# Kernel tuning notes

Measured on AMD Instinct MI355X. Metric: run time of the kernel, lower is better.

The kernel has to match this reference:

```python
import jax, jax.numpy as jnp
import numpy as np

SPATIAL_W = 1.0
INTENSITY_W = 1.0
MAX_ITERS = 100
CONV_THRESH = 1e-4
BOUNDARY = 0.1
NUM_CLASSES = 2
DIRS = ((-1, 0), (1, 0), (0, -1), (0, 1))  # 4-neighborhood


def setup_inputs() -> dict:
    key = jax.random.key(0)
    k1, k2, k3 = jax.random.split(key, 3)
    H = W = 1024
    image = jax.random.uniform(k1, (H, W), dtype=jnp.float32)
    labels = jax.random.randint(k2, (H, W), 1, NUM_CLASSES + 1)
    u = jax.random.uniform(k3, (H, W))
    seeds = jnp.where(u < 0.002, labels, 0).astype(jnp.int32)
    # guarantee both classes present (torch code maps sorted unique labels -> class idx)
    seeds = seeds.at[0, 0].set(1).at[0, 1].set(2)
    return {"image": image, "seeds": seeds}


def _shift(x, di, dj):
    """out[i, j] = x[i+di, j+dj] if in-bounds else 0. Static di, dj in {-1,0,1}."""
    H, W = x.shape[0], x.shape[1]
    pad = [(1, 1), (1, 1)] + [(0, 0)] * (x.ndim - 2)
    xp = jnp.pad(x, pad)
    return xp[1 + di:1 + di + H, 1 + dj:1 + dj + W]


def _transition_stencil(image):
    """Row-normalized 4-neighbor transition weights, [4, H, W].
    Equivalent to the dense NxN matrix P of the torch code restricted to its
    nonzero 4-neighbor stencil."""
    img = image[..., None]  # [H, W, 1] (grayscale -> C=1)
    ones = jnp.ones(image.shape, image.dtype)
    ws = []
    for di, dj in DIRS:
        valid = _shift(ones, di, dj)              # 1 where neighbor in-bounds
        nb = _shift(img, di, dj)                   # neighbor pixel values
        same = ((img > BOUNDARY) ^ (nb > BOUNDARY)).astype(image.dtype)
        diff = img - nb + same
        intensity = jnp.sqrt(jnp.sum(diff * diff, axis=-1))  # per-channel L2 norm
        dist = float(np.sqrt(di * di + dj * dj))  # == 1 for 4-neighborhood
        w = jnp.exp(-SPATIAL_W * dist) * jnp.exp(-INTENSITY_W * intensity) * valid
        ws.append(w)
    ws = jnp.stack(ws)  # [4, H, W]
    rowsum = jnp.sum(ws, axis=0)
    rowsum = jnp.where(rowsum == 0, jnp.ones_like(rowsum), rowsum)
    return ws / rowsum


def reference(image, seeds):
    P = _transition_stencil(image)  # [4, H, W]
    seed_mask = (seeds > 0)[..., None]  # [H, W, 1]
    # one-hot seed probabilities: label l -> class l-1 (sorted unique labels {1,2})
    init = jnp.stack([seeds == l for l in range(1, NUM_CLASSES + 1)],
                     axis=-1).astype(image.dtype)  # [H, W, C]

    def matvec(x):  # (P @ x) as a stencil: x is [H, W, C]
        out = jnp.zeros_like(x)
        for d, (di, dj) in enumerate(DIRS):
            out = out + P[d][..., None] * _shift(x, di, dj)
        return out

    def step(carry, _):
        x, done = carry
        new = jnp.where(seed_mask, init, matvec(x))  # seeds are absorbing
        d = jnp.linalg.norm(new - x)
        new = jnp.where(done, x, new)               # freeze after convergence
        done = done | (d < CONV_THRESH)
        return (new, done), None

    (x, _), _ = jax.lax.scan(step, (init, jnp.array(False)), None, length=MAX_ITERS)
    return x  # [H, W, NUM_CLASSES]
```

## Files before the change

kernel.cpp:

```cpp
#include <hip/hip_runtime.h>
#include <hip/hip_fp16.h>

typedef __attribute__((ext_vector_type(2))) int i32x2;

#define HH 1024
#define ROWP 512
#define NBLK 256
#define TPB 512
#define NSYNC 50
#define BOUNDARY_F 0.1f
#define TOKEN 0x5A5A5A5Au
#define FLAGS_N (NSYNC * NBLK)

union h2u { __half2 h; int i; };

__device__ __forceinline__ i32x2 pack4(float4 v) {
    h2u a, b;
    a.h = __float22half2_rn(make_float2(v.x, v.y));
    b.h = __float22half2_rn(make_float2(v.z, v.w));
    i32x2 r; r.x = a.i; r.y = b.i;
    return r;
}
__device__ __forceinline__ float4 unpack4(i32x2 p) {
    h2u a, b; a.i = p.x; b.i = p.y;
    float2 lo = __half22float2(a.h);
    float2 hi = __half22float2(b.h);
    return make_float4(lo.x, lo.y, hi.x, hi.y);
}

__device__ __forceinline__ void cst8(i32x2* base, int elem, i32x2 val) {
    asm volatile("global_store_dwordx2 %0, %1, %2 sc0 sc1"
                 :: "v"(elem * 8), "v"(val), "s"(base) : "memory");
}
__device__ __forceinline__ i32x2 cld8(const i32x2* base, int elem) {
    i32x2 t;
    asm volatile("global_load_dwordx2 %0, %1, %2 sc0 sc1"
                 : "=v"(t) : "v"(elem * 8), "s"(base) : "memory");
    return t;
}
__device__ __forceinline__ void wait4(i32x2& a, i32x2& b, i32x2& c, i32x2& d) {
    asm volatile("s_waitcnt vmcnt(0)"
                 : "+v"(a), "+v"(b), "+v"(c), "+v"(d) :: "memory");
}
__device__ __forceinline__ void waitvm0() {
    asm volatile("s_waitcnt vmcnt(0)" ::: "memory");
}

__device__ __forceinline__ float wfun(float c, float n, float valid) {
    float same = ((c > BOUNDARY_F) != (n > BOUNDARY_F)) ? 1.0f : 0.0f;
    return valid * __expf(-fabsf(c - n + same));
}

__device__ __forceinline__ float4 stepr(const float* w, bool m0, bool m1,
                                        float4 xc, float4 xu, float4 xd,
                                        float2 xl, float2 xr) {
    float4 o;
    o.x = w[0]*xu.x + w[1]*xd.x + w[2]*xl.x + w[3]*xc.z;
    o.y = w[0]*xu.y + w[1]*xd.y + w[2]*xl.y + w[3]*xc.w;
    o.z = w[4]*xu.z + w[5]*xd.z + w[6]*xc.x + w[7]*xr.x;
    o.w = w[4]*xu.w + w[5]*xd.w + w[6]*xc.y + w[7]*xr.y;
    if (m0) { o.x = xc.x; o.y = xc.y; }
    if (m1) { o.z = xc.z; o.w = xc.w; }
    return o;
}

__device__ __forceinline__ void horiz(const float4* row, int tid, float4 xc,
                                      float2* xl, float2* xr) {
    const float2* r2 = (const float2*)row;
    *xl = (tid > 0) ? r2[2 * tid - 1] : make_float2(xc.x, xc.y);
    *xr = (tid < ROWP - 1) ? r2[2 * tid + 2] : make_float2(xc.z, xc.w);
}

__global__ void rw_init_kernel(unsigned* __restrict__ flags) {
    int g = blockIdx.x * blockDim.x + threadIdx.x;
    if (g < FLAGS_N) flags[g] = 0u;
}

__launch_bounds__(TPB)
__global__ void rw_persist_kernel(const float* __restrict__ img,
                                  const int* __restrict__ seeds,
                                  float4* __restrict__ out4,
                                  i32x2* __restrict__ parE,
                                  i32x2* __restrict__ parO,
                                  unsigned* __restrict__ flags) {
    const int tid = threadIdx.x;
    const int blk = blockIdx.x;
    const int band = ((blk & 7) << 5) | (blk >> 3);
    const int i0 = band * 4;

    __shared__ float4 srows[10][ROWP];

    float cfv[6][8];
    unsigned mb0 = 0, mb1 = 0;
    float4 s0, s1, s2, s3;
    {
        const float2* img2 = (const float2*)img;
        const int2* seeds2 = (const int2*)seeds;
#pragma unroll
        for (int L = 0; L < 6; ++L) {
            const int g = min(max(i0 - 1 + L, 0), HH - 1);
            const int P = g * ROWP + tid;
            const int p = P * 2;
            const int j = p & 1023;
            const int uP = (g > 0) ? P - ROWP : P;
            const int dP = (g < HH - 1) ? P + ROWP : P;
            const int lp = (j > 0) ? p - 1 : p;
            const int rp = (j < 1022) ? p + 2 : p + 1;

            float2 cc = img2[P], iu = img2[uP], id = img2[dP];
            float il = img[lp], ir = img[rp];
            const float vU = (g > 0) ? 1.0f : 0.0f;
            const float vD = (g < HH - 1) ? 1.0f : 0.0f;
            const float vL = (j > 0) ? 1.0f : 0.0f;
            const float vR = (j < 1022) ? 1.0f : 0.0f;

            float w0u = wfun(cc.x, iu.x, vU), w0d = wfun(cc.x, id.x, vD);
            float w0l = wfun(cc.x, il, vL),   w0r = wfun(cc.x, cc.y, 1.0f);
            float rs0 = w0u + w0d + w0l + w0r;
            float inv0 = (rs0 > 0.0f) ? 1.0f / rs0 : 0.0f;
            float w1u = wfun(cc.y, iu.y, vU), w1d = wfun(cc.y, id.y, vD);
            float w1l = wfun(cc.y, cc.x, 1.0f), w1r = wfun(cc.y, ir, vR);
            float rs1 = w1u + w1d + w1l + w1r;
            float inv1 = (rs1 > 0.0f) ? 1.0f / rs1 : 0.0f;

            cfv[L][0] = w0u * inv0; cfv[L][1] = w0d * inv0;
            cfv[L][2] = w0l * inv0; cfv[L][3] = w0r * inv0;
            cfv[L][4] = w1u * inv1; cfv[L][5] = w1d * inv1;
            cfv[L][6] = w1l * inv1; cfv[L][7] = w1r * inv1;

            int2 s = seeds2[P];
            if (s.x > 0) mb0 |= 1u << L;
            if (s.y > 0) mb1 |= 1u << L;
            if (L >= 1 && L <= 4) {
                float4 v;
                v.x = (s.x == 1) ? 1.0f : 0.0f;
                v.y = (s.x == 2) ? 1.0f : 0.0f;
                v.z = (s.y == 1) ? 1.0f : 0.0f;
                v.w = (s.y == 2) ? 1.0f : 0.0f;
                if (L == 1) s0 = v; else if (L == 2) s1 = v;
                else if (L == 3) s2 = v; else s3 = v;
            }
        }
    }

    srows[1][tid] = s0; srows[2][tid] = s1;
    srows[3][tid] = s2; srows[4][tid] = s3;
    cst8(parE, (i0 + 0) * ROWP + tid, pack4(s0));
    cst8(parE, (i0 + 1) * ROWP + tid, pack4(s1));
    cst8(parE, (i0 + 2) * ROWP + tid, pack4(s2));
    cst8(parE, (i0 + 3) * ROWP + tid, pack4(s3));
    waitvm0();
    __syncthreads();
    if (tid == 0)
        __hip_atomic_store(&flags[band], TOKEN, __ATOMIC_RELAXED,
                           __HIP_MEMORY_SCOPE_AGENT);

    const int gU2 = max(i0 - 2, 0), gU1 = max(i0 - 1, 0);
    const int gD0 = min(i0 + 4, HH - 1), gD1 = min(i0 + 5, HH - 1);

    for (int m = 0; m < NSYNC; ++m) {
        if (tid == 0 && band > 0) {
            int guard = 0;
            while (__hip_atomic_load(&flags[m * NBLK + band - 1], __ATOMIC_RELAXED,
                                     __HIP_MEMORY_SCOPE_AGENT) != TOKEN) {
                if (++guard > (1 << 22)) break;
            }
        }
        if (tid == 64 && band < NBLK - 1) {
            int guard = 0;
            while (__hip_atomic_load(&flags[m * NBLK + band + 1], __ATOMIC_RELAXED,
                                     __HIP_MEMORY_SCOPE_AGENT) != TOKEN) {
                if (++guard > (1 << 22)) break;
            }
        }
        __syncthreads();
        asm volatile("" ::: "memory");

        const i32x2* pin = (m & 1) ? parO : parE;

        i32x2 rA = cld8(pin, gU2 * ROWP + tid);
        i32x2 rB = cld8(pin, gU1 * ROWP + tid);
        i32x2 rC = cld8(pin, gD0 * ROWP + tid);
        i32x2 rD = cld8(pin, gD1 * ROWP + tid);

        float2 xl, xr;
        horiz(&srows[2][0], tid, s1, &xl, &xr);
        float4 y2 = stepr(cfv[2], (mb0 >> 2) & 1, (mb1 >> 2) & 1, s1, s0, s2, xl, xr);
        horiz(&srows[3][0], tid, s2, &xl, &xr);
        float4 y3 = stepr(cfv[3], (mb0 >> 3) & 1, (mb1 >> 3) & 1, s2, s1, s3, xl, xr);
        srows[7][tid] = y2;
        srows[8][tid] = y3;

        wait4(rA, rB, rC, rD);
        float4 vU2 = unpack4(rA);
        float4 vU1 = unpack4(rB);
        float4 vD0 = unpack4(rC);
        float4 vD1 = unpack4(rD);
        srows[0][tid] = vU1;
        srows[5][tid] = vD0;
        __syncthreads();

        horiz(&srows[0][0], tid, vU1, &xl, &xr);
        float4 y0 = stepr(cfv[0], (mb0 >> 0) & 1, (mb1 >> 0) & 1, vU1, vU2, s0, xl, xr);
        horiz(&srows[1][0], tid, s0, &xl, &xr);
        float4 y1 = stepr(cfv[1], (mb0 >> 1) & 1, (mb1 >> 1) & 1, s0, vU1, s1, xl, xr);
        horiz(&srows[4][0], tid, s3, &xl, &xr);
        float4 y4 = stepr(cfv[4], (mb0 >> 4) & 1, (mb1 >> 4) & 1, s3, s2, vD0, xl, xr);
        horiz(&srows[5][0], tid, vD0, &xl, &xr);
        float4 y5 = stepr(cfv[5], (mb0 >> 5) & 1, (mb1 >> 5) & 1, vD0, s3, vD1, xl, xr);
        srows[6][tid] = y1;
        srows[9][tid] = y4;
        __syncthreads();

        i32x2* pout = (m & 1) ? parE : parO;
        const bool last = (m == NSYNC - 1);

        horiz(&srows[6][0], tid, y1, &xl, &xr);
        float4 o0 = stepr(cfv[1], (mb0 >> 1) & 1, (mb1 >> 1) & 1, y1, y0, y2, xl, xr);
        if (!last) cst8(pout, (i0 + 0) * ROWP + tid, pack4(o0));
        horiz(&srows[7][0], tid, y2, &xl, &xr);
        float4 o1 = stepr(cfv[2], (mb0 >> 2) & 1, (mb1 >> 2) & 1, y2, y1, y3, xl, xr);
        if (!last) cst8(pout, (i0 + 1) * ROWP + tid, pack4(o1));
        horiz(&srows[8][0], tid, y3, &xl, &xr);
        float4 o2 = stepr(cfv[3], (mb0 >> 3) & 1, (mb1 >> 3) & 1, y3, y2, y4, xl, xr);
        if (!last) cst8(pout, (i0 + 2) * ROWP + tid, pack4(o2));
        horiz(&srows[9][0], tid, y4, &xl, &xr);
        float4 o3 = stepr(cfv[4], (mb0 >> 4) & 1, (mb1 >> 4) & 1, y4, y3, y5, xl, xr);
        if (!last) cst8(pout, (i0 + 3) * ROWP + tid, pack4(o3));

        if (last) {
            out4[(i0 + 0) * ROWP + tid] = o0;
            out4[(i0 + 1) * ROWP + tid] = o1;
            out4[(i0 + 2) * ROWP + tid] = o2;
            out4[(i0 + 3) * ROWP + tid] = o3;
            break;
        }

        waitvm0();
        __syncthreads();
        if (tid == 0)
            __hip_atomic_store(&flags[(m + 1) * NBLK + band], TOKEN,
                               __ATOMIC_RELAXED, __HIP_MEMORY_SCOPE_AGENT);

        srows[1][tid] = o0; srows[2][tid] = o1;
        srows[3][tid] = o2; srows[4][tid] = o3;
        s0 = o0; s1 = o1; s2 = o2; s3 = o3;
    }
}

extern "C" void kernel_launch(void* const* d_in, const int* in_sizes, int n_in,
                              void* d_out, int out_size, void* d_ws, size_t ws_size,
                              hipStream_t stream) {
    const float* img = (const float*)d_in[0];
    const int* seeds = (const int*)d_in[1];

    float4* out4 = (float4*)d_out;
    char* ws = (char*)d_ws;
    i32x2* parE = (i32x2*)ws;
    i32x2* parO = (i32x2*)(ws + 4ull * 1024 * 1024);
    unsigned* flags = (unsigned*)(ws + 8ull * 1024 * 1024);

    rw_init_kernel<<<(FLAGS_N + 255) / 256, 256, 0, stream>>>(flags);
    rw_persist_kernel<<<NBLK, TPB, 0, stream>>>(img, seeds, out4, parE, parO, flags);
}
```

Measured before the change: 240.6 us.

## Deepen temporal blocking to four steps per inter-block sync with wider halo

Each block now loads a 4-row halo above and below its band and advances four Jacobi steps per exchange instead of two, which halves the number of inter-block flag synchronisations from 50 to 25. The goal is to cut the global sync and halo round-trip latency that dominates the persistent kernel. In exchange it does redundant halo computation (more stencil rows per sync), uses more registers for ten coefficient rows, and needs extra shared memory and barriers per round.

```diff
diff --git a/kernel.cpp b/kernel.cpp
--- a/kernel.cpp
+++ b/kernel.cpp
@@ -7,7 +7,7 @@
 #define ROWP 512
 #define NBLK 256
 #define TPB 512
-#define NSYNC 50
+#define NSYNC 25
 #define BOUNDARY_F 0.1f
 #define TOKEN 0x5A5A5A5Au
 #define FLAGS_N (NSYNC * NBLK)
@@ -38,9 +38,11 @@
                  : "=v"(t) : "v"(elem * 8), "s"(base) : "memory");
     return t;
 }
-__device__ __forceinline__ void wait4(i32x2& a, i32x2& b, i32x2& c, i32x2& d) {
+__device__ __forceinline__ void wait8(i32x2& a, i32x2& b, i32x2& c, i32x2& d,
+                                      i32x2& e, i32x2& f, i32x2& g, i32x2& h) {
     asm volatile("s_waitcnt vmcnt(0)"
-                 : "+v"(a), "+v"(b), "+v"(c), "+v"(d) :: "memory");
+                 : "+v"(a), "+v"(b), "+v"(c), "+v"(d),
+                   "+v"(e), "+v"(f), "+v"(g), "+v"(h) :: "memory");
 }
 __device__ __forceinline__ void waitvm0() {
     asm volatile("s_waitcnt vmcnt(0)" ::: "memory");
@@ -88,17 +90,18 @@
     const int band = ((blk & 7) << 5) | (blk >> 3);
     const int i0 = band * 4;
 
-    __shared__ float4 srows[10][ROWP];
-
-    float cfv[6][8];
+    __shared__ float4 bufA[10][ROWP];
+    __shared__ float4 bufB[8][ROWP];
+
+    float cfv[10][8];
     unsigned mb0 = 0, mb1 = 0;
     float4 s0, s1, s2, s3;
     {
         const float2* img2 = (const float2*)img;
         const int2* seeds2 = (const int2*)seeds;
 #pragma unroll
-        for (int L = 0; L < 6; ++L) {
-            const int g = min(max(i0 - 1 + L, 0), HH - 1);
+        for (int L = 1; L <= 10; ++L) {
+            const int g = min(max(i0 - 4 + L, 0), HH - 1);
             const int P = g * ROWP + tid;
             const int p = P * 2;
             const int j = p & 1023;
@@ -123,28 +126,28 @@
             float rs1 = w1u + w1d + w1l + w1r;
             float inv1 = (rs1 > 0.0f) ? 1.0f / rs1 : 0.0f;
 
-            cfv[L][0] = w0u * inv0; cfv[L][1] = w0d * inv0;
-            cfv[L][2] = w0l * inv0; cfv[L][3] = w0r * inv0;
-            cfv[L][4] = w1u * inv1; cfv[L][5] = w1d * inv1;
-            cfv[L][6] = w1l * inv1; cfv[L][7] = w1r * inv1;
+            cfv[L-1][0] = w0u * inv0; cfv[L-1][1] = w0d * inv0;
+            cfv[L-1][2] = w0l * inv0; cfv[L-1][3] = w0r * inv0;
+            cfv[L-1][4] = w1u * inv1; cfv[L-1][5] = w1d * inv1;
+            cfv[L-1][6] = w1l * inv1; cfv[L-1][7] = w1r * inv1;
 
             int2 s = seeds2[P];
             if (s.x > 0) mb0 |= 1u << L;
             if (s.y > 0) mb1 |= 1u << L;
-            if (L >= 1 && L <= 4) {
+            if (L >= 4 && L <= 7) {
                 float4 v;
                 v.x = (s.x == 1) ? 1.0f : 0.0f;
                 v.y = (s.x == 2) ? 1.0f : 0.0f;
                 v.z = (s.y == 1) ? 1.0f : 0.0f;
                 v.w = (s.y == 2) ? 1.0f : 0.0f;
-                if (L == 1) s0 = v; else if (L == 2) s1 = v;
-                else if (L == 3) s2 = v; else s3 = v;
+                if (L == 4) s0 = v; else if (L == 5) s1 = v;
+                else if (L == 6) s2 = v; else s3 = v;
             }
         }
     }
 
-    srows[1][tid] = s0; srows[2][tid] = s1;
-    srows[3][tid] = s2; srows[4][tid] = s3;
+    bufA[3][tid] = s0; bufA[4][tid] = s1;
+    bufA[5][tid] = s2; bufA[6][tid] = s3;
     cst8(parE, (i0 + 0) * ROWP + tid, pack4(s0));
     cst8(parE, (i0 + 1) * ROWP + tid, pack4(s1));
     cst8(parE, (i0 + 2) * ROWP + tid, pack4(s2));
@@ -155,8 +158,10 @@
         __hip_atomic_store(&flags[band], TOKEN, __ATOMIC_RELAXED,
                            __HIP_MEMORY_SCOPE_AGENT);
 
-    const int gU2 = max(i0 - 2, 0), gU1 = max(i0 - 1, 0);
+    const int gU0 = max(i0 - 4, 0), gU1 = max(i0 - 3, 0);
+    const int gU2 = max(i0 - 2, 0), gU3 = max(i0 - 1, 0);
     const int gD0 = min(i0 + 4, HH - 1), gD1 = min(i0 + 5, HH - 1);
+    const int gD2 = min(i0 + 6, HH - 1), gD3 = min(i0 + 7, HH - 1);
 
     for (int m = 0; m < NSYNC; ++m) {
         if (tid == 0 && band > 0) {
@@ -178,54 +183,106 @@
 
         const i32x2* pin = (m & 1) ? parO : parE;
 
-        i32x2 rA = cld8(pin, gU2 * ROWP + tid);
+        i32x2 rA = cld8(pin, gU0 * ROWP + tid);
         i32x2 rB = cld8(pin, gU1 * ROWP + tid);
-        i32x2 rC = cld8(pin, gD0 * ROWP + tid);
-        i32x2 rD = cld8(pin, gD1 * ROWP + tid);
+        i32x2 rC = cld8(pin, gU2 * ROWP + tid);
+        i32x2 rD = cld8(pin, gU3 * ROWP + tid);
+        i32x2 rE = cld8(pin, gD0 * ROWP + tid);
+        i32x2 rF = cld8(pin, gD1 * ROWP + tid);
+        i32x2 rG = cld8(pin, gD2 * ROWP + tid);
+        i32x2 rH = cld8(pin, gD3 * ROWP + tid);
 
         float2 xl, xr;
-        horiz(&srows[2][0], tid, s1, &xl, &xr);
-        float4 y2 = stepr(cfv[2], (mb0 >> 2) & 1, (mb1 >> 2) & 1, s1, s0, s2, xl, xr);
-        horiz(&srows[3][0], tid, s2, &xl, &xr);
-        float4 y3 = stepr(cfv[3], (mb0 >> 3) & 1, (mb1 >> 3) & 1, s2, s1, s3, xl, xr);
-        srows[7][tid] = y2;
-        srows[8][tid] = y3;
-
-        wait4(rA, rB, rC, rD);
-        float4 vU2 = unpack4(rA);
-        float4 vU1 = unpack4(rB);
-        float4 vD0 = unpack4(rC);
-        float4 vD1 = unpack4(rD);
-        srows[0][tid] = vU1;
-        srows[5][tid] = vD0;
-        __syncthreads();
-
-        horiz(&srows[0][0], tid, vU1, &xl, &xr);
-        float4 y0 = stepr(cfv[0], (mb0 >> 0) & 1, (mb1 >> 0) & 1, vU1, vU2, s0, xl, xr);
-        horiz(&srows[1][0], tid, s0, &xl, &xr);
-        float4 y1 = stepr(cfv[1], (mb0 >> 1) & 1, (mb1 >> 1) & 1, s0, vU1, s1, xl, xr);
-        horiz(&srows[4][0], tid, s3, &xl, &xr);
-        float4 y4 = stepr(cfv[4], (mb0 >> 4) & 1, (mb1 >> 4) & 1, s3, s2, vD0, xl, xr);
-        horiz(&srows[5][0], tid, vD0, &xl, &xr);
-        float4 y5 = stepr(cfv[5], (mb0 >> 5) & 1, (mb1 >> 5) & 1, vD0, s3, vD1, xl, xr);
-        srows[6][tid] = y1;
-        srows[9][tid] = y4;
+        horiz(&bufA[4][0], tid, s1, &xl, &xr);
+        float4 y1_5 = stepr(cfv[4], (mb0 >> 5) & 1, (mb1 >> 5) & 1, s1, s0, s2, xl, xr);
+        horiz(&bufA[5][0], tid, s2, &xl, &xr);
+        float4 y1_6 = stepr(cfv[5], (mb0 >> 6) & 1, (mb1 >> 6) & 1, s2, s1, s3, xl, xr);
+        bufB[3][tid] = y1_5;
+        bufB[4][tid] = y1_6;
+
+        wait8(rA, rB, rC, rD, rE, rF, rG, rH);
+        float4 x0_0  = unpack4(rA);
+        float4 x0_1  = unpack4(rB);
+        float4 x0_2  = unpack4(rC);
+        float4 x0_3  = unpack4(rD);
+        float4 x0_8  = unpack4(rE);
+        float4 x0_9  = unpack4(rF);
+        float4 x0_10 = unpack4(rG);
+        float4 x0_11 = unpack4(rH);
+        bufA[0][tid] = x0_1; bufA[1][tid] = x0_2; bufA[2][tid] = x0_3;
+        bufA[7][tid] = x0_8; bufA[8][tid] = x0_9; bufA[9][tid] = x0_10;
+        __syncthreads();
+
+        horiz(&bufA[0][0], tid, x0_1, &xl, &xr);
+        float4 y1_1 = stepr(cfv[0], (mb0 >> 1) & 1, (mb1 >> 1) & 1, x0_1, x0_0, x0_2, xl, xr);
+        horiz(&bufA[1][0], tid, x0_2, &xl, &xr);
+        float4 y1_2 = stepr(cfv[1], (mb0 >> 2) & 1, (mb1 >> 2) & 1, x0_2, x0_1, x0_3, xl, xr);
+        horiz(&bufA[2][0], tid, x0_3, &xl, &xr);
+        float4 y1_3 = stepr(cfv[2], (mb0 >> 3) & 1, (mb1 >> 3) & 1, x0_3, x0_2, s0, xl, xr);
+        horiz(&bufA[3][0], tid, s0, &xl, &xr);
+        float4 y1_4 = stepr(cfv[3], (mb0 >> 4) & 1, (mb1 >> 4) & 1, s0, x0_3, s1, xl, xr);
+        horiz(&bufA[6][0], tid, s3, &xl, &xr);
+        float4 y1_7 = stepr(cfv[6], (mb0 >> 7) & 1, (mb1 >> 7) & 1, s3, s2, x0_8, xl, xr);
+        horiz(&bufA[7][0], tid, x0_8, &xl, &xr);
+        float4 y1_8 = stepr(cfv[7], (mb0 >> 8) & 1, (mb1 >> 8) & 1, x0_8, s3, x0_9, xl, xr);
+        horiz(&bufA[8][0], tid, x0_9, &xl, &xr);
+        float4 y1_9 = stepr(cfv[8], (mb0 >> 9) & 1, (mb1 >> 9) & 1, x0_9, x0_8, x0_10, xl, xr);
+        horiz(&bufA[9][0], tid, x0_10, &xl, &xr);
+        float4 y1_10 = stepr(cfv[9], (mb0 >> 10) & 1, (mb1 >> 10) & 1, x0_10, x0_9, x0_11, xl, xr);
+        bufB[0][tid] = y1_2; bufB[1][tid] = y1_3; bufB[2][tid] = y1_4;
+        bufB[5][tid] = y1_7; bufB[6][tid] = y1_8; bufB[7][tid] = y1_9;
+        __syncthreads();
+
+        horiz(&bufB[0][0], tid, y1_2, &xl, &xr);
+        float4 y2_2 = stepr(cfv[1], (mb0 >> 2) & 1, (mb1 >> 2) & 1, y1_2, y1_1, y1_3, xl, xr);
+        horiz(&bufB[1][0], tid, y1_3, &xl, &xr);
+        float4 y2_3 = stepr(cfv[2], (mb0 >> 3) & 1, (mb1 >> 3) & 1, y1_3, y1_2, y1_4, xl, xr);
+        horiz(&bufB[2][0], tid, y1_4, &xl, &xr);
+        float4 y2_4 = stepr(cfv[3], (mb0 >> 4) & 1, (mb1 >> 4) & 1, y1_4, y1_3, y1_5, xl, xr);
+        horiz(&bufB[3][0], tid, y1_5, &xl, &xr);
+        float4 y2_5 = stepr(cfv[4], (mb0 >> 5) & 1, (mb1 >> 5) & 1, y1_5, y1_4, y1_6, xl, xr);
+        horiz(&bufB[4][0], tid, y1_6, &xl, &xr);
+        float4 y2_6 = stepr(cfv[5], (mb0 >> 6) & 1, (mb1 >> 6) & 1, y1_6, y1_5, y1_7, xl, xr);
+        horiz(&bufB[5][0], tid, y1_7, &xl, &xr);
+        float4 y2_7 = stepr(cfv[6], (mb0 >> 7) & 1, (mb1 >> 7) & 1, y1_7, y1_6, y1_8, xl, xr);
+        horiz(&bufB[6][0], tid, y1_8, &xl, &xr);
+        float4 y2_8 = stepr(cfv[7], (mb0 >> 8) & 1, (mb1 >> 8) & 1, y1_8, y1_7, y1_9, xl, xr);
+        horiz(&bufB[7][0], tid, y1_9, &xl, &xr);
+        float4 y2_9 = stepr(cfv[8], (mb0 >> 9) & 1, (mb1 >> 9) & 1, y1_9, y1_8, y1_10, xl, xr);
+        bufA[0][tid] = y2_3; bufA[1][tid] = y2_4; bufA[2][tid] = y2_5;
+        bufA[3][tid] = y2_6; bufA[4][tid] = y2_7; bufA[5][tid] = y2_8;
+        __syncthreads();
+
+        horiz(&bufA[0][0], tid, y2_3, &xl, &xr);
+        float4 y3_3 = stepr(cfv[2], (mb0 >> 3) & 1, (mb1 >> 3) & 1, y2_3, y2_2, y2_4, xl, xr);
+        horiz(&bufA[1][0], tid, y2_4, &xl, &xr);
+        float4 y3_4 = stepr(cfv[3], (mb0 >> 4) & 1, (mb1 >> 4) & 1, y2_4, y2_3, y2_5, xl, xr);
+        horiz(&bufA[2][0], tid, y2_5, &xl, &xr);
+        float4 y3_5 = stepr(cfv[4], (mb0 >> 5) & 1, (mb1 >> 5) & 1, y2_5, y2_4, y2_6, xl, xr);
+        horiz(&bufA[3][0], tid, y2_6, &xl, &xr);
+        float4 y3_6 = stepr(cfv[5], (mb0 >> 6) & 1, (mb1 >> 6) & 1, y2_6, y2_5, y2_7, xl, xr);
+        horiz(&bufA[4][0], tid, y2_7, &xl, &xr);
+        float4 y3_7 = stepr(cfv[6], (mb0 >> 7) & 1, (mb1 >> 7) & 1, y2_7, y2_6, y2_8, xl, xr);
+        horiz(&bufA[5][0], tid, y2_8, &xl, &xr);
+        float4 y3_8 = stepr(cfv[7], (mb0 >> 8) & 1, (mb1 >> 8) & 1, y2_8, y2_7, y2_9, xl, xr);
+        bufB[0][tid] = y3_4; bufB[1][tid] = y3_5;
+        bufB[2][tid] = y3_6; bufB[3][tid] = y3_7;
         __syncthreads();
 
         i32x2* pout = (m & 1) ? parE : parO;
         const bool last = (m == NSYNC - 1);
 
-        horiz(&srows[6][0], tid, y1, &xl, &xr);
-        float4 o0 = stepr(cfv[1], (mb0 >> 1) & 1, (mb1 >> 1) & 1, y1, y0, y2, xl, xr);
+        horiz(&bufB[0][0], tid, y3_4, &xl, &xr);
+        float4 o0 = stepr(cfv[3], (mb0 >> 4) & 1, (mb1 >> 4) & 1, y3_4, y3_3, y3_5, xl, xr);
         if (!last) cst8(pout, (i0 + 0) * ROWP + tid, pack4(o0));
-        horiz(&srows[7][0], tid, y2, &xl, &xr);
-        float4 o1 = stepr(cfv[2], (mb0 >> 2) & 1, (mb1 >> 2) & 1, y2, y1, y3, xl, xr);
+        horiz(&bufB[1][0], tid, y3_5, &xl, &xr);
+        float4 o1 = stepr(cfv[4], (mb0 >> 5) & 1, (mb1 >> 5) & 1, y3_5, y3_4, y3_6, xl, xr);
         if (!last) cst8(pout, (i0 + 1) * ROWP + tid, pack4(o1));
-        horiz(&srows[8][0], tid, y3, &xl, &xr);
-        float4 o2 = stepr(cfv[3], (mb0 >> 3) & 1, (mb1 >> 3) & 1, y3, y2, y4, xl, xr);
+        horiz(&bufB[2][0], tid, y3_6, &xl, &xr);
+        float4 o2 = stepr(cfv[5], (mb0 >> 6) & 1, (mb1 >> 6) & 1, y3_6, y3_5, y3_7, xl, xr);
         if (!last) cst8(pout, (i0 + 2) * ROWP + tid, pack4(o2));
-        horiz(&srows[9][0], tid, y4, &xl, &xr);
-        float4 o3 = stepr(cfv[4], (mb0 >> 4) & 1, (mb1 >> 4) & 1, y4, y3, y5, xl, xr);
+        horiz(&bufB[3][0], tid, y3_7, &xl, &xr);
+        float4 o3 = stepr(cfv[6], (mb0 >> 7) & 1, (mb1 >> 7) & 1, y3_7, y3_6, y3_8, xl, xr);
         if (!last) cst8(pout, (i0 + 3) * ROWP + tid, pack4(o3));
 
         if (last) {
@@ -242,8 +299,8 @@
             __hip_atomic_store(&flags[(m + 1) * NBLK + band], TOKEN,
                                __ATOMIC_RELAXED, __HIP_MEMORY_SCOPE_AGENT);
 
-        srows[1][tid] = o0; srows[2][tid] = o1;
-        srows[3][tid] = o2; srows[4][tid] = o3;
+        bufA[3][tid] = o0; bufA[4][tid] = o1;
+        bufA[5][tid] = o2; bufA[6][tid] = o3;
         s0 = o0; s1 = o1; s2 = o2; s3 = o3;
     }
 }
```

After: 365.2 us. +51.8%, slower.

## Deepen temporal blocking to four steps per global sync with wavefront schedule

Applied to the files above, without the earlier changes.

Each block now exchanges a 4-row halo on each side and advances four Jacobi steps per inter-block synchronization instead of two, halving the number of global flag handshakes. The redundant halo rows are computed in a staggered wavefront through rotating shared-memory buffers. To keep register pressure manageable, the per-pixel transition weights are stored packed as fp16, and the right/left weight is recomputed from the row-sum-to-one identity. This adds redundant halo compute, more barriers per sync, and extra fp16 rounding of the coefficients.

```diff
diff --git a/kernel.cpp b/kernel.cpp
--- a/kernel.cpp
+++ b/kernel.cpp
@@ -7,7 +7,7 @@
 #define ROWP 512
 #define NBLK 256
 #define TPB 512
-#define NSYNC 50
+#define NSYNC 25
 #define BOUNDARY_F 0.1f
 #define TOKEN 0x5A5A5A5Au
 #define FLAGS_N (NSYNC * NBLK)
@@ -27,6 +27,13 @@
     float2 hi = __half22float2(b.h);
     return make_float4(lo.x, lo.y, hi.x, hi.y);
 }
+__device__ __forceinline__ unsigned packh2(float a, float b) {
+    h2u u; u.h = __float22half2_rn(make_float2(a, b));
+    return (unsigned)u.i;
+}
+__device__ __forceinline__ float2 uph2(unsigned u) {
+    h2u x; x.i = (int)u; return __half22float2(x.h);
+}
 
 __device__ __forceinline__ void cst8(i32x2* base, int elem, i32x2 val) {
     asm volatile("global_store_dwordx2 %0, %1, %2 sc0 sc1"
@@ -38,9 +45,11 @@
                  : "=v"(t) : "v"(elem * 8), "s"(base) : "memory");
     return t;
 }
-__device__ __forceinline__ void wait4(i32x2& a, i32x2& b, i32x2& c, i32x2& d) {
+__device__ __forceinline__ void wait8(i32x2& a, i32x2& b, i32x2& c, i32x2& d,
+                                      i32x2& e, i32x2& f, i32x2& g, i32x2& h) {
     asm volatile("s_waitcnt vmcnt(0)"
-                 : "+v"(a), "+v"(b), "+v"(c), "+v"(d) :: "memory");
+                 : "+v"(a), "+v"(b), "+v"(c), "+v"(d),
+                   "+v"(e), "+v"(f), "+v"(g), "+v"(h) :: "memory");
 }
 __device__ __forceinline__ void waitvm0() {
     asm volatile("s_waitcnt vmcnt(0)" ::: "memory");
@@ -51,14 +60,19 @@
     return valid * __expf(-fabsf(c - n + same));
 }
 
-__device__ __forceinline__ float4 stepr(const float* w, bool m0, bool m1,
+__device__ __forceinline__ float4 stepw(const unsigned* cwr, bool m0, bool m1,
                                         float4 xc, float4 xu, float4 xd,
                                         float2 xl, float2 xr) {
+    float2 ud0 = uph2(cwr[0]);
+    float2 lr  = uph2(cwr[1]);
+    float2 ud1 = uph2(cwr[2]);
+    float w0r = 1.0f - ud0.x - ud0.y - lr.x;
+    float w1l = 1.0f - ud1.x - ud1.y - lr.y;
     float4 o;
-    o.x = w[0]*xu.x + w[1]*xd.x + w[2]*xl.x + w[3]*xc.z;
-    o.y = w[0]*xu.y + w[1]*xd.y + w[2]*xl.y + w[3]*xc.w;
-    o.z = w[4]*xu.z + w[5]*xd.z + w[6]*xc.x + w[7]*xr.x;
-    o.w = w[4]*xu.w + w[5]*xd.w + w[6]*xc.y + w[7]*xr.y;
+    o.x = ud0.x*xu.x + ud0.y*xd.x + lr.x*xl.x + w0r*xc.z;
+    o.y = ud0.x*xu.y + ud0.y*xd.y + lr.x*xl.y + w0r*xc.w;
+    o.z = ud1.x*xu.z + ud1.y*xd.z + w1l*xc.x + lr.y*xr.x;
+    o.w = ud1.x*xu.w + ud1.y*xd.w + w1l*xc.y + lr.y*xr.y;
     if (m0) { o.x = xc.x; o.y = xc.y; }
     if (m1) { o.z = xc.z; o.w = xc.w; }
     return o;
@@ -88,17 +102,20 @@
     const int band = ((blk & 7) << 5) | (blk >> 3);
     const int i0 = band * 4;
 
-    __shared__ float4 srows[10][ROWP];
-
-    float cfv[6][8];
+    __shared__ float4 X [10][ROWP];
+    __shared__ float4 R1[3][ROWP];
+    __shared__ float4 R2[3][ROWP];
+    __shared__ float4 R3[3][ROWP];
+
+    unsigned cw[10][3];
     unsigned mb0 = 0, mb1 = 0;
-    float4 s0, s1, s2, s3;
+    float4 xr4, xr5, xr6, xr7;
     {
         const float2* img2 = (const float2*)img;
         const int2* seeds2 = (const int2*)seeds;
 #pragma unroll
-        for (int L = 0; L < 6; ++L) {
-            const int g = min(max(i0 - 1 + L, 0), HH - 1);
+        for (int L = 1; L <= 10; ++L) {
+            const int g = min(max(i0 - 4 + L, 0), HH - 1);
             const int P = g * ROWP + tid;
             const int p = P * 2;
             const int j = p & 1023;
@@ -123,40 +140,48 @@
             float rs1 = w1u + w1d + w1l + w1r;
             float inv1 = (rs1 > 0.0f) ? 1.0f / rs1 : 0.0f;
 
-            cfv[L][0] = w0u * inv0; cfv[L][1] = w0d * inv0;
-            cfv[L][2] = w0l * inv0; cfv[L][3] = w0r * inv0;
-            cfv[L][4] = w1u * inv1; cfv[L][5] = w1d * inv1;
-            cfv[L][6] = w1l * inv1; cfv[L][7] = w1r * inv1;
+            cw[L-1][0] = packh2(w0u * inv0, w0d * inv0);
+            cw[L-1][1] = packh2(w0l * inv0, w1r * inv1);
+            cw[L-1][2] = packh2(w1u * inv1, w1d * inv1);
 
             int2 s = seeds2[P];
             if (s.x > 0) mb0 |= 1u << L;
             if (s.y > 0) mb1 |= 1u << L;
-            if (L >= 1 && L <= 4) {
+            if (L >= 4 && L <= 7) {
                 float4 v;
                 v.x = (s.x == 1) ? 1.0f : 0.0f;
                 v.y = (s.x == 2) ? 1.0f : 0.0f;
                 v.z = (s.y == 1) ? 1.0f : 0.0f;
                 v.w = (s.y == 2) ? 1.0f : 0.0f;
-                if (L == 1) s0 = v; else if (L == 2) s1 = v;
-                else if (L == 3) s2 = v; else s3 = v;
+                if (L == 4) xr4 = v; else if (L == 5) xr5 = v;
+                else if (L == 6) xr6 = v; else xr7 = v;
             }
         }
     }
 
-    srows[1][tid] = s0; srows[2][tid] = s1;
-    srows[3][tid] = s2; srows[4][tid] = s3;
-    cst8(parE, (i0 + 0) * ROWP + tid, pack4(s0));
-    cst8(parE, (i0 + 1) * ROWP + tid, pack4(s1));
-    cst8(parE, (i0 + 2) * ROWP + tid, pack4(s2));
-    cst8(parE, (i0 + 3) * ROWP + tid, pack4(s3));
+    X[3][tid] = xr4; X[4][tid] = xr5;
+    X[5][tid] = xr6; X[6][tid] = xr7;
+    cst8(parE, (i0 + 0) * ROWP + tid, pack4(xr4));
+    cst8(parE, (i0 + 1) * ROWP + tid, pack4(xr5));
+    cst8(parE, (i0 + 2) * ROWP + tid, pack4(xr6));
+    cst8(parE, (i0 + 3) * ROWP + tid, pack4(xr7));
     waitvm0();
     __syncthreads();
     if (tid == 0)
         __hip_atomic_store(&flags[band], TOKEN, __ATOMIC_RELAXED,
                            __HIP_MEMORY_SCOPE_AGENT);
 
-    const int gU2 = max(i0 - 2, 0), gU1 = max(i0 - 1, 0);
+    const int gU0 = max(i0 - 4, 0), gU1 = max(i0 - 3, 0);
+    const int gU2 = max(i0 - 2, 0), gU3 = max(i0 - 1, 0);
     const int gD0 = min(i0 + 4, HH - 1), gD1 = min(i0 + 5, HH - 1);
+    const int gD2 = min(i0 + 6, HH - 1), gD3 = min(i0 + 7, HH - 1);
+
+#define HUPD(dst, CWI, BIT, xc_, xu_, xd_, SLOT) do {                        \
+        float2 xl_, xr_;                                                     \
+        horiz(&SLOT[0], tid, xc_, &xl_, &xr_);                               \
+        dst = stepw(cw[CWI], (mb0 >> (BIT)) & 1, (mb1 >> (BIT)) & 1,         \
+                    xc_, xu_, xd_, xl_, xr_);                                \
+    } while (0)
 
     for (int m = 0; m < NSYNC; ++m) {
         if (tid == 0 && band > 0) {
@@ -178,57 +203,81 @@
 
         const i32x2* pin = (m & 1) ? parO : parE;
 
-        i32x2 rA = cld8(pin, gU2 * ROWP + tid);
+        i32x2 rA = cld8(pin, gU0 * ROWP + tid);
         i32x2 rB = cld8(pin, gU1 * ROWP + tid);
-        i32x2 rC = cld8(pin, gD0 * ROWP + tid);
-        i32x2 rD = cld8(pin, gD1 * ROWP + tid);
-
-        float2 xl, xr;
-        horiz(&srows[2][0], tid, s1, &xl, &xr);
-        float4 y2 = stepr(cfv[2], (mb0 >> 2) & 1, (mb1 >> 2) & 1, s1, s0, s2, xl, xr);
-        horiz(&srows[3][0], tid, s2, &xl, &xr);
-        float4 y3 = stepr(cfv[3], (mb0 >> 3) & 1, (mb1 >> 3) & 1, s2, s1, s3, xl, xr);
-        srows[7][tid] = y2;
-        srows[8][tid] = y3;
-
-        wait4(rA, rB, rC, rD);
-        float4 vU2 = unpack4(rA);
-        float4 vU1 = unpack4(rB);
-        float4 vD0 = unpack4(rC);
-        float4 vD1 = unpack4(rD);
-        srows[0][tid] = vU1;
-        srows[5][tid] = vD0;
-        __syncthreads();
-
-        horiz(&srows[0][0], tid, vU1, &xl, &xr);
-        float4 y0 = stepr(cfv[0], (mb0 >> 0) & 1, (mb1 >> 0) & 1, vU1, vU2, s0, xl, xr);
-        horiz(&srows[1][0], tid, s0, &xl, &xr);
-        float4 y1 = stepr(cfv[1], (mb0 >> 1) & 1, (mb1 >> 1) & 1, s0, vU1, s1, xl, xr);
-        horiz(&srows[4][0], tid, s3, &xl, &xr);
-        float4 y4 = stepr(cfv[4], (mb0 >> 4) & 1, (mb1 >> 4) & 1, s3, s2, vD0, xl, xr);
-        horiz(&srows[5][0], tid, vD0, &xl, &xr);
-        float4 y5 = stepr(cfv[5], (mb0 >> 5) & 1, (mb1 >> 5) & 1, vD0, s3, vD1, xl, xr);
-        srows[6][tid] = y1;
-        srows[9][tid] = y4;
-        __syncthreads();
-
-        i32x2* pout = (m & 1) ? parE : parO;
-        const bool last = (m == NSYNC - 1);
-
-        horiz(&srows[6][0], tid, y1, &xl, &xr);
-        float4 o0 = stepr(cfv[1], (mb0 >> 1) & 1, (mb1 >> 1) & 1, y1, y0, y2, xl, xr);
-        if (!last) cst8(pout, (i0 + 0) * ROWP + tid, pack4(o0));
-        horiz(&srows[7][0], tid, y2, &xl, &xr);
-        float4 o1 = stepr(cfv[2], (mb0 >> 2) & 1, (mb1 >> 2) & 1, y2, y1, y3, xl, xr);
-        if (!last) cst8(pout, (i0 + 1) * ROWP + tid, pack4(o1));
-        horiz(&srows[8][0], tid, y3, &xl, &xr);
-        float4 o2 = stepr(cfv[3], (mb0 >> 3) & 1, (mb1 >> 3) & 1, y3, y2, y4, xl, xr);
-        if (!last) cst8(pout, (i0 + 2) * ROWP + tid, pack4(o2));
-        horiz(&srows[9][0], tid, y4, &xl, &xr);
-        float4 o3 = stepr(cfv[4], (mb0 >> 4) & 1, (mb1 >> 4) & 1, y4, y3, y5, xl, xr);
-        if (!last) cst8(pout, (i0 + 3) * ROWP + tid, pack4(o3));
-
-        if (last) {
+        i32x2 rC = cld8(pin, gU2 * ROWP + tid);
+        i32x2 rD = cld8(pin, gU3 * ROWP + tid);
+        i32x2 rE = cld8(pin, gD0 * ROWP + tid);
+        i32x2 rF = cld8(pin, gD1 * ROWP + tid);
+        i32x2 rG = cld8(pin, gD2 * ROWP + tid);
+        i32x2 rH = cld8(pin, gD3 * ROWP + tid);
+
+        float4 y1_5, y1_6;
+        HUPD(y1_5, 4, 5, xr5, xr4, xr6, X[4]);
+        HUPD(y1_6, 5, 6, xr6, xr5, xr7, X[5]);
+
+        wait8(rA, rB, rC, rD, rE, rF, rG, rH);
+        float4 xr0  = unpack4(rA);
+        float4 xr1  = unpack4(rB);
+        float4 xr2  = unpack4(rC);
+        float4 xr3  = unpack4(rD);
+        float4 xr8  = unpack4(rE);
+        float4 xr9  = unpack4(rF);
+        float4 xr10 = unpack4(rG);
+        float4 xr11 = unpack4(rH);
+        X[0][tid] = xr1; X[1][tid] = xr2; X[2][tid] = xr3;
+        X[7][tid] = xr8; X[8][tid] = xr9; X[9][tid] = xr10;
+        __syncthreads();
+
+        float4 y1_1, y1_2, y1_3, y1_4, y1_7, y1_8, y1_9, y1_10;
+        float4 y2_2, y2_3, y2_4, y2_5, y2_6, y2_7, y2_8, y2_9;
+        float4 y3_3, y3_4, y3_5, y3_6, y3_7, y3_8;
+        float4 o0, o1, o2, o3;
+
+        HUPD(y1_1, 0, 1, xr1, xr0, xr2, X[0]);
+        HUPD(y1_2, 1, 2, xr2, xr1, xr3, X[1]);
+        R1[2][tid] = y1_2;
+        __syncthreads();
+        HUPD(y1_3, 2, 3, xr3, xr2, xr4, X[2]);
+        HUPD(y2_2, 1, 2, y1_2, y1_1, y1_3, R1[2]);
+        R1[0][tid] = y1_3;
+        __syncthreads();
+        HUPD(y1_4, 3, 4, xr4, xr3, xr5, X[3]);
+        HUPD(y2_3, 2, 3, y1_3, y1_2, y1_4, R1[0]);
+        R1[1][tid] = y1_4; R2[0][tid] = y2_3;
+        __syncthreads();
+        HUPD(y2_4, 3, 4, y1_4, y1_3, y1_5, R1[1]);
+        HUPD(y3_3, 2, 3, y2_3, y2_2, y2_4, R2[0]);
+        R1[2][tid] = y1_5; R2[1][tid] = y2_4;
+        __syncthreads();
+        HUPD(y2_5, 4, 5, y1_5, y1_4, y1_6, R1[2]);
+        HUPD(y3_4, 3, 4, y2_4, y2_3, y2_5, R2[1]);
+        R1[0][tid] = y1_6; R2[2][tid] = y2_5; R3[1][tid] = y3_4;
+        __syncthreads();
+        HUPD(y1_7, 6, 7, xr7, xr6, xr8, X[6]);
+        HUPD(y2_6, 5, 6, y1_6, y1_5, y1_7, R1[0]);
+        HUPD(y3_5, 4, 5, y2_5, y2_4, y2_6, R2[2]);
+        HUPD(o0,   3, 4, y3_4, y3_3, y3_5, R3[1]);
+        R1[1][tid] = y1_7; R2[0][tid] = y2_6; R3[2][tid] = y3_5;
+        __syncthreads();
+        HUPD(y1_8, 7, 8, xr8, xr7, xr9, X[7]);
+        HUPD(y2_7, 6, 7, y1_7, y1_6, y1_8, R1[1]);
+        HUPD(y3_6, 5, 6, y2_6, y2_5, y2_7, R2[0]);
+        HUPD(o1,   4, 5, y3_5, y3_4, y3_6, R3[2]);
+        R1[2][tid] = y1_8; R2[1][tid] = y2_7; R3[0][tid] = y3_6;
+        __syncthreads();
+        HUPD(y1_9, 8, 9, xr9, xr8, xr10, X[8]);
+        HUPD(y2_8, 7, 8, y1_8, y1_7, y1_9, R1[2]);
+        HUPD(y3_7, 6, 7, y2_7, y2_6, y2_8, R2[1]);
+        HUPD(o2,   5, 6, y3_6, y3_5, y3_7, R3[0]);
+        R1[0][tid] = y1_9; R2[2][tid] = y2_8; R3[1][tid] = y3_7;
+        __syncthreads();
+        HUPD(y1_10, 9, 10, xr10, xr9, xr11, X[9]);
+        HUPD(y2_9, 8, 9, y1_9, y1_8, y1_10, R1[0]);
+        HUPD(y3_8, 7, 8, y2_8, y2_7, y2_9, R2[2]);
+        HUPD(o3,   6, 7, y3_7, y3_6, y3_8, R3[1]);
+
+        if (m == NSYNC - 1) {
             out4[(i0 + 0) * ROWP + tid] = o0;
             out4[(i0 + 1) * ROWP + tid] = o1;
             out4[(i0 + 2) * ROWP + tid] = o2;
@@ -236,16 +285,22 @@
             break;
         }
 
+        i32x2* pout = (m & 1) ? parE : parO;
+        cst8(pout, (i0 + 0) * ROWP + tid, pack4(o0));
+        cst8(pout, (i0 + 1) * ROWP + tid, pack4(o1));
+        cst8(pout, (i0 + 2) * ROWP + tid, pack4(o2));
+        cst8(pout, (i0 + 3) * ROWP + tid, pack4(o3));
         waitvm0();
         __syncthreads();
         if (tid == 0)
             __hip_atomic_store(&flags[(m + 1) * NBLK + band], TOKEN,
                                __ATOMIC_RELAXED, __HIP_MEMORY_SCOPE_AGENT);
 
-        srows[1][tid] = o0; srows[2][tid] = o1;
-        srows[3][tid] = o2; srows[4][tid] = o3;
-        s0 = o0; s1 = o1; s2 = o2; s3 = o3;
+        X[3][tid] = o0; X[4][tid] = o1;
+        X[5][tid] = o2; X[6][tid] = o3;
+        xr4 = o0; xr5 = o1; xr6 = o2; xr7 = o3;
     }
+#undef HUPD
 }
 
 extern "C" void kernel_launch(void* const* d_in, const int* in_sizes, int n_in,
```

Result: slower. 468.0 us (+94.5%).

## Replace block barrier flag signaling with per-wave byte flags and fetch halo neighbors directly

Applied to the files above, without the earlier changes.

Each wavefront now writes its own byte in an 8-byte flag after draining its stores, which removes the __syncthreads before signaling. Neighbor bands poll both 4-byte halves with a pipelined inline-asm loop. The horizontal neighbors of halo rows are loaded straight from global memory, and partial sums for the interior edge rows are computed before the halo arrives, which drops one LDS barrier per iteration. This trades extra global loads and more complex asm for shorter synchronization latency on the critical path, and it depends on byte-store and dword-load coherence for correctness.

```diff
diff --git a/kernel.cpp b/kernel.cpp
--- a/kernel.cpp
+++ b/kernel.cpp
@@ -9,7 +9,7 @@
 #define TPB 512
 #define NSYNC 50
 #define BOUNDARY_F 0.1f
-#define TOKEN 0x5A5A5A5Au
+#define TOKB 0x5A
 #define FLAGS_N (NSYNC * NBLK)
 
 union h2u { __half2 h; int i; };
@@ -27,6 +27,9 @@
     float2 hi = __half22float2(b.h);
     return make_float4(lo.x, lo.y, hi.x, hi.y);
 }
+__device__ __forceinline__ float2 uph2(int u) {
+    h2u x; x.i = u; return __half22float2(x.h);
+}
 
 __device__ __forceinline__ void cst8(i32x2* base, int elem, i32x2 val) {
     asm volatile("global_store_dwordx2 %0, %1, %2 sc0 sc1"
@@ -38,12 +41,61 @@
                  : "=v"(t) : "v"(elem * 8), "s"(base) : "memory");
     return t;
 }
-__device__ __forceinline__ void wait4(i32x2& a, i32x2& b, i32x2& c, i32x2& d) {
+__device__ __forceinline__ int cld4b(const void* base, int byteoff) {
+    int t;
+    asm volatile("global_load_dword %0, %1, %2 sc0 sc1"
+                 : "=v"(t) : "v"(byteoff), "s"(base) : "memory");
+    return t;
+}
+__device__ __forceinline__ void cstb(void* base, int byteoff, int val) {
+    asm volatile("global_store_byte %0, %1, %2 sc0 sc1"
+                 :: "v"(byteoff), "v"(val), "s"(base) : "memory");
+}
+__device__ __forceinline__ void wait8m(i32x2& a, i32x2& b, i32x2& c, i32x2& d,
+                                       int& e, int& f, int& g, int& h) {
+    asm volatile("s_waitcnt vmcnt(0)"
+                 : "+v"(a), "+v"(b), "+v"(c), "+v"(d),
+                   "+v"(e), "+v"(f), "+v"(g), "+v"(h) :: "memory");
+}
+__device__ __forceinline__ void drain4(int& a, int& b, int& c, int& d) {
     asm volatile("s_waitcnt vmcnt(0)"
                  : "+v"(a), "+v"(b), "+v"(c), "+v"(d) :: "memory");
 }
-__device__ __forceinline__ void waitvm0() {
-    asm volatile("s_waitcnt vmcnt(0)" ::: "memory");
+
+__device__ __forceinline__ void poll8(const void* base, int byteoff,
+                                      int& a0, int& b0, int& a1, int& b1) {
+    unsigned gt;
+    asm volatile(
+        "global_load_dword %[a0], %[off], %[srd] sc0 sc1\n\t"
+        "global_load_dword %[b0], %[off4], %[srd] sc0 sc1\n\t"
+        "global_load_dword %[a1], %[off], %[srd] sc0 sc1\n\t"
+        "global_load_dword %[b1], %[off4], %[srd] sc0 sc1\n\t"
+        "s_movk_i32 %[g], 0x7fff\n\t"
+        "Lp%=:\n\t"
+        "s_waitcnt vmcnt(2)\n\t"
+        "v_cmp_eq_u32 vcc, 0x5a5a5a5a, %[a0]\n\t"
+        "s_cbranch_vccz Lr0%=\n\t"
+        "v_cmp_eq_u32 vcc, 0x5a5a5a5a, %[b0]\n\t"
+        "s_cbranch_vccnz Ld%=\n\t"
+        "Lr0%=:\n\t"
+        "global_load_dword %[a0], %[off], %[srd] sc0 sc1\n\t"
+        "global_load_dword %[b0], %[off4], %[srd] sc0 sc1\n\t"
+        "s_sub_i32 %[g], %[g], 1\n\t"
+        "s_cmp_lt_i32 %[g], 1\n\t"
+        "s_cbranch_scc1 Ld%=\n\t"
+        "s_waitcnt vmcnt(2)\n\t"
+        "v_cmp_eq_u32 vcc, 0x5a5a5a5a, %[a1]\n\t"
+        "s_cbranch_vccz Lr1%=\n\t"
+        "v_cmp_eq_u32 vcc, 0x5a5a5a5a, %[b1]\n\t"
+        "s_cbranch_vccnz Ld%=\n\t"
+        "Lr1%=:\n\t"
+        "global_load_dword %[a1], %[off], %[srd] sc0 sc1\n\t"
+        "global_load_dword %[b1], %[off4], %[srd] sc0 sc1\n\t"
+        "s_branch Lp%=\n\t"
+        "Ld%=:\n\t"
+        : [a0]"+v"(a0), [b0]"+v"(b0), [a1]"+v"(a1), [b1]"+v"(b1), [g]"=&s"(gt)
+        : [off]"v"(byteoff), [off4]"v"(byteoff + 4), [srd]"s"(base)
+        : "vcc", "memory");
 }
 
 __device__ __forceinline__ float wfun(float c, float n, float valid) {
@@ -63,6 +115,42 @@
     if (m1) { o.z = xc.z; o.w = xc.w; }
     return o;
 }
+__device__ __forceinline__ float4 part_noxu(const float* w, float4 xc, float4 xd,
+                                            float2 xl, float2 xr) {
+    float4 p;
+    p.x = w[1]*xd.x + w[2]*xl.x + w[3]*xc.z;
+    p.y = w[1]*xd.y + w[2]*xl.y + w[3]*xc.w;
+    p.z = w[5]*xd.z + w[6]*xc.x + w[7]*xr.x;
+    p.w = w[5]*xd.w + w[6]*xc.y + w[7]*xr.y;
+    return p;
+}
+__device__ __forceinline__ float4 fin_xu(const float* w, bool m0, bool m1,
+                                         float4 p, float4 xu, float4 xc) {
+    float4 o;
+    o.x = p.x + w[0]*xu.x;  o.y = p.y + w[0]*xu.y;
+    o.z = p.z + w[4]*xu.z;  o.w = p.w + w[4]*xu.w;
+    if (m0) { o.x = xc.x; o.y = xc.y; }
+    if (m1) { o.z = xc.z; o.w = xc.w; }
+    return o;
+}
+__device__ __forceinline__ float4 part_noxd(const float* w, float4 xc, float4 xu,
+                                            float2 xl, float2 xr) {
+    float4 p;
+    p.x = w[0]*xu.x + w[2]*xl.x + w[3]*xc.z;
+    p.y = w[0]*xu.y + w[2]*xl.y + w[3]*xc.w;
+    p.z = w[4]*xu.z + w[6]*xc.x + w[7]*xr.x;
+    p.w = w[4]*xu.w + w[6]*xc.y + w[7]*xr.y;
+    return p;
+}
+__device__ __forceinline__ float4 fin_xd(const float* w, bool m0, bool m1,
+                                         float4 p, float4 xd, float4 xc) {
+    float4 o;
+    o.x = p.x + w[1]*xd.x;  o.y = p.y + w[1]*xd.y;
+    o.z = p.z + w[5]*xd.z;  o.w = p.w + w[5]*xd.w;
+    if (m0) { o.x = xc.x; o.y = xc.y; }
+    if (m1) { o.z = xc.z; o.w = xc.w; }
+    return o;
+}
 
 __device__ __forceinline__ void horiz(const float4* row, int tid, float4 xc,
                                       float2* xl, float2* xr) {
@@ -73,7 +161,7 @@
 
 __global__ void rw_init_kernel(unsigned* __restrict__ flags) {
     int g = blockIdx.x * blockDim.x + threadIdx.x;
-    if (g < FLAGS_N) flags[g] = 0u;
+    if (g < FLAGS_N * 2) flags[g] = 0u;
 }
 
 __launch_bounds__(TPB)
@@ -82,13 +170,13 @@
                                   float4* __restrict__ out4,
                                   i32x2* __restrict__ parE,
                                   i32x2* __restrict__ parO,
-                                  unsigned* __restrict__ flags) {
+                                  unsigned long long* __restrict__ flags8) {
     const int tid = threadIdx.x;
     const int blk = blockIdx.x;
     const int band = ((blk & 7) << 5) | (blk >> 3);
     const int i0 = band * 4;
 
-    __shared__ float4 srows[10][ROWP];
+    __shared__ float4 S[8][ROWP];
 
     float cfv[6][8];
     unsigned mb0 = 0, mb1 = 0;
@@ -143,88 +231,90 @@
         }
     }
 
-    srows[1][tid] = s0; srows[2][tid] = s1;
-    srows[3][tid] = s2; srows[4][tid] = s3;
+    int qa0 = 0, qb0 = 0, qa1 = 0, qb1 = 0;
+
+    S[0][tid] = s0; S[1][tid] = s1;
+    S[2][tid] = s2; S[3][tid] = s3;
     cst8(parE, (i0 + 0) * ROWP + tid, pack4(s0));
     cst8(parE, (i0 + 1) * ROWP + tid, pack4(s1));
     cst8(parE, (i0 + 2) * ROWP + tid, pack4(s2));
     cst8(parE, (i0 + 3) * ROWP + tid, pack4(s3));
-    waitvm0();
-    __syncthreads();
-    if (tid == 0)
-        __hip_atomic_store(&flags[band], TOKEN, __ATOMIC_RELAXED,
-                           __HIP_MEMORY_SCOPE_AGENT);
+    drain4(qa0, qb0, qa1, qb1);
+    if ((tid & 63) == 0)
+        cstb((void*)flags8, band * 8 + (tid >> 6), TOKB);
 
     const int gU2 = max(i0 - 2, 0), gU1 = max(i0 - 1, 0);
     const int gD0 = min(i0 + 4, HH - 1), gD1 = min(i0 + 5, HH - 1);
+    const int eU1 = gU1 * ROWP, eD0 = gD0 * ROWP;
+    const int offBl = (tid > 0)        ? (eU1 + tid) * 8 - 4   : eU1 * 8;
+    const int offBr = (tid < ROWP - 1) ? (eU1 + tid + 1) * 8   : (eU1 + tid) * 8;
+    const int offCl = (tid > 0)        ? (eD0 + tid) * 8 - 4   : eD0 * 8;
+    const int offCr = (tid < ROWP - 1) ? (eD0 + tid + 1) * 8   : (eD0 + tid) * 8;
 
     for (int m = 0; m < NSYNC; ++m) {
-        if (tid == 0 && band > 0) {
-            int guard = 0;
-            while (__hip_atomic_load(&flags[m * NBLK + band - 1], __ATOMIC_RELAXED,
-                                     __HIP_MEMORY_SCOPE_AGENT) != TOKEN) {
-                if (++guard > (1 << 22)) break;
-            }
-        }
-        if (tid == 64 && band < NBLK - 1) {
-            int guard = 0;
-            while (__hip_atomic_load(&flags[m * NBLK + band + 1], __ATOMIC_RELAXED,
-                                     __HIP_MEMORY_SCOPE_AGENT) != TOKEN) {
-                if (++guard > (1 << 22)) break;
-            }
-        }
+        if (band > 0 && tid == 0)
+            poll8((const void*)flags8, (m * NBLK + band - 1) * 8,
+                  qa0, qb0, qa1, qb1);
+        if (band < NBLK - 1 && tid == 64)
+            poll8((const void*)flags8, (m * NBLK + band + 1) * 8,
+                  qa0, qb0, qa1, qb1);
         __syncthreads();
         asm volatile("" ::: "memory");
 
         const i32x2* pin = (m & 1) ? parO : parE;
 
         i32x2 rA = cld8(pin, gU2 * ROWP + tid);
-        i32x2 rB = cld8(pin, gU1 * ROWP + tid);
-        i32x2 rC = cld8(pin, gD0 * ROWP + tid);
+        i32x2 rB = cld8(pin, eU1 + tid);
+        i32x2 rC = cld8(pin, eD0 + tid);
         i32x2 rD = cld8(pin, gD1 * ROWP + tid);
+        int hBl = cld4b(pin, offBl);
+        int hBr = cld4b(pin, offBr);
+        int hCl = cld4b(pin, offCl);
+        int hCr = cld4b(pin, offCr);
 
         float2 xl, xr;
-        horiz(&srows[2][0], tid, s1, &xl, &xr);
+        horiz(&S[1][0], tid, s1, &xl, &xr);
         float4 y2 = stepr(cfv[2], (mb0 >> 2) & 1, (mb1 >> 2) & 1, s1, s0, s2, xl, xr);
-        horiz(&srows[3][0], tid, s2, &xl, &xr);
+        horiz(&S[2][0], tid, s2, &xl, &xr);
         float4 y3 = stepr(cfv[3], (mb0 >> 3) & 1, (mb1 >> 3) & 1, s2, s1, s3, xl, xr);
-        srows[7][tid] = y2;
-        srows[8][tid] = y3;
-
-        wait4(rA, rB, rC, rD);
+        S[5][tid] = y2;
+        S[6][tid] = y3;
+        horiz(&S[0][0], tid, s0, &xl, &xr);
+        float4 p1 = part_noxu(cfv[1], s0, s1, xl, xr);
+        horiz(&S[3][0], tid, s3, &xl, &xr);
+        float4 p4 = part_noxd(cfv[4], s3, s2, xl, xr);
+
+        wait8m(rA, rB, rC, rD, hBl, hBr, hCl, hCr);
         float4 vU2 = unpack4(rA);
         float4 vU1 = unpack4(rB);
         float4 vD0 = unpack4(rC);
         float4 vD1 = unpack4(rD);
-        srows[0][tid] = vU1;
-        srows[5][tid] = vD0;
-        __syncthreads();
-
-        horiz(&srows[0][0], tid, vU1, &xl, &xr);
-        float4 y0 = stepr(cfv[0], (mb0 >> 0) & 1, (mb1 >> 0) & 1, vU1, vU2, s0, xl, xr);
-        horiz(&srows[1][0], tid, s0, &xl, &xr);
-        float4 y1 = stepr(cfv[1], (mb0 >> 1) & 1, (mb1 >> 1) & 1, s0, vU1, s1, xl, xr);
-        horiz(&srows[4][0], tid, s3, &xl, &xr);
-        float4 y4 = stepr(cfv[4], (mb0 >> 4) & 1, (mb1 >> 4) & 1, s3, s2, vD0, xl, xr);
-        horiz(&srows[5][0], tid, vD0, &xl, &xr);
-        float4 y5 = stepr(cfv[5], (mb0 >> 5) & 1, (mb1 >> 5) & 1, vD0, s3, vD1, xl, xr);
-        srows[6][tid] = y1;
-        srows[9][tid] = y4;
+
+        float4 y1 = fin_xu(cfv[1], (mb0 >> 1) & 1, (mb1 >> 1) & 1, p1, vU1, s0);
+        float4 y4 = fin_xd(cfv[4], (mb0 >> 4) & 1, (mb1 >> 4) & 1, p4, vD0, s3);
+        float2 bl = (tid > 0)        ? uph2(hBl) : make_float2(vU1.x, vU1.y);
+        float2 br = (tid < ROWP - 1) ? uph2(hBr) : make_float2(vU1.z, vU1.w);
+        float4 y0 = stepr(cfv[0], (mb0 >> 0) & 1, (mb1 >> 0) & 1, vU1, vU2, s0, bl, br);
+        float2 cl = (tid > 0)        ? uph2(hCl) : make_float2(vD0.x, vD0.y);
+        float2 cr = (tid < ROWP - 1) ? uph2(hCr) : make_float2(vD0.z, vD0.w);
+        float4 y5 = stepr(cfv[5], (mb0 >> 5) & 1, (mb1 >> 5) & 1, vD0, s3, vD1, cl, cr);
+        S[4][tid] = y1;
+        S[7][tid] = y4;
         __syncthreads();
 
         i32x2* pout = (m & 1) ? parE : parO;
         const bool last = (m == NSYNC - 1);
 
-        horiz(&srows[6][0], tid, y1, &xl, &xr);
+        horiz(&S[4][0], tid, y1, &xl, &xr);
         float4 o0 = stepr(cfv[1], (mb0 >> 1) & 1, (mb1 >> 1) & 1, y1, y0, y2, xl, xr);
         if (!last) cst8(pout, (i0 + 0) * ROWP + tid, pack4(o0));
-        horiz(&srows[7][0], tid, y2, &xl, &xr);
+        horiz(&S[5][0], tid, y2, &xl, &xr);
         float4 o1 = stepr(cfv[2], (mb0 >> 2) & 1, (mb1 >> 2) & 1, y2, y1, y3, xl, xr);
         if (!last) cst8(pout, (i0 + 1) * ROWP + tid, pack4(o1));
-        horiz(&srows[8][0], tid, y3, &xl, &xr);
+        horiz(&S[6][0], tid, y3, &xl, &xr);
         float4 o2 = stepr(cfv[3], (mb0 >> 3) & 1, (mb1 >> 3) & 1, y3, y2, y4, xl, xr);
         if (!last) cst8(pout, (i0 + 2) * ROWP + tid, pack4(o2));
-        horiz(&srows[9][0], tid, y4, &xl, &xr);
+        horiz(&S[7][0], tid, y4, &xl, &xr);
         float4 o3 = stepr(cfv[4], (mb0 >> 4) & 1, (mb1 >> 4) & 1, y4, y3, y5, xl, xr);
         if (!last) cst8(pout, (i0 + 3) * ROWP + tid, pack4(o3));
 
@@ -233,17 +323,16 @@
             out4[(i0 + 1) * ROWP + tid] = o1;
             out4[(i0 + 2) * ROWP + tid] = o2;
             out4[(i0 + 3) * ROWP + tid] = o3;
+            drain4(qa0, qb0, qa1, qb1);
             break;
         }
 
-        waitvm0();
-        __syncthreads();
-        if (tid == 0)
-            __hip_atomic_store(&flags[(m + 1) * NBLK + band], TOKEN,
-                               __ATOMIC_RELAXED, __HIP_MEMORY_SCOPE_AGENT);
-
-        srows[1][tid] = o0; srows[2][tid] = o1;
-        srows[3][tid] = o2; srows[4][tid] = o3;
+        drain4(qa0, qb0, qa1, qb1);
+        if ((tid & 63) == 0)
+            cstb((void*)flags8, ((m + 1) * NBLK + band) * 8 + (tid >> 6), TOKB);
+
+        S[0][tid] = o0; S[1][tid] = o1;
+        S[2][tid] = o2; S[3][tid] = o3;
         s0 = o0; s1 = o1; s2 = o2; s3 = o3;
     }
 }
@@ -258,8 +347,9 @@
     char* ws = (char*)d_ws;
     i32x2* parE = (i32x2*)ws;
     i32x2* parO = (i32x2*)(ws + 4ull * 1024 * 1024);
-    unsigned* flags = (unsigned*)(ws + 8ull * 1024 * 1024);
-
-    rw_init_kernel<<<(FLAGS_N + 255) / 256, 256, 0, stream>>>(flags);
-    rw_persist_kernel<<<NBLK, TPB, 0, stream>>>(img, seeds, out4, parE, parO, flags);
-}
+    unsigned long long* flags8 =
+        (unsigned long long*)(ws + 8ull * 1024 * 1024);
+
+    rw_init_kernel<<<(FLAGS_N * 2 + 255) / 256, 256, 0, stream>>>((unsigned*)flags8);
+    rw_persist_kernel<<<NBLK, TPB, 0, stream>>>(img, seeds, out4, parE, parO, flags8);
+}
```

After: 611.0 us. 154% more time.
